# Performance work log

Hardware: AMD Instinct MI355X
Metric: run time of the kernel (lower is better)

## Reference

```python
import jax, jax.numpy as jnp
import numpy as np

B_SZ, T, IN_DIM, N_STATES, OUT_DIM = 64, 1024, 256, 512, 256


def setup_inputs() -> dict:
    key = jax.random.key(0)
    ks = jax.random.split(key, 5)
    def g(k, shp, sc):
        return jax.random.normal(k, shp, dtype=jnp.float32) * sc
    return {
        "x": g(ks[0], (B_SZ, T, IN_DIM), 1.0),
        "A": g(ks[1], (N_STATES, N_STATES), 1.0 / np.sqrt(N_STATES)),
        "Bm": g(ks[2], (IN_DIM, N_STATES), 1.0 / np.sqrt(IN_DIM)),
        "b": jnp.zeros((N_STATES,), jnp.float32),
        "C": g(ks[3], (N_STATES, OUT_DIM), 1.0 / np.sqrt(N_STATES)),
        "c": jnp.zeros((OUT_DIM,), jnp.float32),
        "D": g(ks[4], (N_STATES, OUT_DIM), 1.0 / np.sqrt(N_STATES)),
        "d": jnp.zeros((OUT_DIM,), jnp.float32),
    }


def reference(x, A, Bm, b, C, c, D, d):
    # x: [B, T, IN] -> time-major [T, B, IN] (mirrors tf.transpose perm=[1,0,2])
    xT = jnp.transpose(x, (1, 0, 2))
    s0 = jnp.zeros((x.shape[0], A.shape[0]), x.dtype)  # get_init_state: zeros [B, num_states]

    def step(state, xt):
        # nonlinear SSM cell: state update + Gaussian output params
        new_state = jnp.tanh(xt @ Bm + state @ A + b)
        loc = new_state @ C + c
        scale = jax.nn.softplus(new_state @ D + d)  # scale_diag > 0
        # emit stacked [2, B, OUT] (loc, scale) and the PRE-update state
        return new_state, (jnp.stack([loc, scale], axis=0), state)

    _, (ys, prev_states) = jax.lax.scan(step, s0, xT)
    # ys: [T, 2, B, OUT] -> [2, B, T, OUT] (tf perm [1,2,0,3])
    outputs = jnp.transpose(ys, (1, 2, 0, 3))
    state_out = prev_states[-1]  # state before the last cell update
    return outputs, state_out
```

## Files before the change

kernel.cpp:

```cpp
#include <hip/hip_runtime.h>
#include <hip/hip_bf16.h>
#include <cstdint>


typedef _Float16 f16;
typedef _Float16 f16x2 __attribute__((ext_vector_type(2)));
typedef _Float16 f16x4 __attribute__((ext_vector_type(4)));
typedef _Float16 f16x8 __attribute__((ext_vector_type(8)));
typedef float    f32x4 __attribute__((ext_vector_type(4)));

#define NS 512

#define OFF_S16   (0ull)
#define OFF_X16   (0ull)
#define OFF_U16   (67108864ull)
#define OFF_BMT   (134217728ull)
#define OFF_CDT   (134479872ull)
#define OFF_APREP (135004160ull)
#define OFF_ASTR  (135397376ull)

#if defined(__has_builtin)
#  if __has_builtin(__builtin_amdgcn_fdot2)
#    define HAS_FDOT2 1
#  endif
#endif

__device__ __forceinline__ float fdot2f(unsigned a, unsigned s, float c) {
#ifdef HAS_FDOT2
  return __builtin_amdgcn_fdot2(__builtin_bit_cast(f16x2, a),
                                __builtin_bit_cast(f16x2, s), c, false);
#else
  f16x2 av = __builtin_bit_cast(f16x2, a);
  f16x2 sv = __builtin_bit_cast(f16x2, s);
  return c + (float)av[0] * (float)sv[0] + (float)av[1] * (float)sv[1];
#endif
}

__device__ __forceinline__ unsigned packh2(float a, float b) {
  f16x2 h; h[0] = (f16)a; h[1] = (f16)b;
  return __builtin_bit_cast(unsigned, h);
}


__global__ void ck_x(const float* __restrict__ xg, f16* __restrict__ x16) {
  int i = (blockIdx.x * 256 + threadIdx.x) * 4;
  float4 v = *(const float4*)(xg + i);
  f16x4 h; h[0] = (f16)v.x; h[1] = (f16)v.y; h[2] = (f16)v.z; h[3] = (f16)v.w;
  *(f16x4*)(x16 + i) = h;
}

__global__ void ck_bmt(const float* __restrict__ Bm, f16* __restrict__ BmT) {
  int g = blockIdx.x * 256 + threadIdx.x;
  int n = g >> 8, k = g & 255;
  BmT[g] = (f16)Bm[k * 512 + n];
}

__global__ void ck_cdt(const float* __restrict__ C, const float* __restrict__ D,
                       f16* __restrict__ CDT) {
  int g = blockIdx.x * 256 + threadIdx.x;
  int n = g >> 9, k = g & 511;
  float v = (n < 256) ? C[k * 256 + n] : D[k * 256 + (n - 256)];
  CDT[g] = (f16)v;
}

__global__ void ck_a(const float* __restrict__ Ag, unsigned* __restrict__ Aprep,
                     unsigned* __restrict__ Astr) {
  int g = blockIdx.x * 256 + threadIdx.x;
  if (g < 98304) {
    int t = g / 192, rr = g % 192;
    int p = rr >> 3, jj = rr & 7;
    int kb = t >> 6, l = t & 63;
    int r0 = kb * 64 + 2 * p;
    int j = jj * 64 + l;
    Aprep[g] = packh2(Ag[r0 * 512 + j], Ag[(r0 + 1) * 512 + j]);
  } else {
    int q = g - 98304;
    int F = q >> 2, d = q & 3;
    int t = F & 511, f = F >> 9;
    int pp = f >> 1, jj2 = f & 1;
    int jj = jj2 * 4 + d;
    int kb = t >> 6, l = t & 63;
    int r0 = kb * 64 + 48 + 2 * pp;
    int j = jj * 64 + l;
    Astr[q] = packh2(Ag[r0 * 512 + j], Ag[(r0 + 1) * 512 + j]);
  }
}

template <int KDIM, int MODE>
__global__ __launch_bounds__(256, 2) void gemm_kernel(
    const f16* __restrict__ Ag, const f16* __restrict__ Bt,
    const float* __restrict__ bias0, const float* __restrict__ bias1,
    void* __restrict__ outp) {
  __shared__ f16 At[128 * 40];
  __shared__ f16 Bs[128 * 40];
  const int tid = threadIdx.x;
  const int m0 = blockIdx.y * 128;
  const int n0 = blockIdx.x * 128;
  const int w = tid >> 6, lane = tid & 63;
  const int wm = w & 1, wn = w >> 1;
  const int r = lane & 15, qd = lane >> 4;

  f32x4 zero4 = {0.f, 0.f, 0.f, 0.f};
  f32x4 acc[4][4];
#pragma unroll
  for (int mt = 0; mt < 4; ++mt)
#pragma unroll
    for (int nt = 0; nt < 4; ++nt) acc[mt][nt] = zero4;

  for (int kk = 0; kk < KDIM; kk += 32) {
#pragma unroll
    for (int s = 0; s < 2; ++s) {
      int fi = tid * 2 + s;
      int row = fi >> 2, q = fi & 3;
      float4 av = *(const float4*)(Ag + (size_t)(m0 + row) * KDIM + kk + q * 8);
      *(float4*)(At + row * 40 + q * 8) = av;
      float4 bv = *(const float4*)(Bt + (size_t)(n0 + row) * KDIM + kk + q * 8);
      *(float4*)(Bs + row * 40 + q * 8) = bv;
    }
    __syncthreads();
    f16x8 af[4], bf[4];
#pragma unroll
    for (int mt = 0; mt < 4; ++mt)
      af[mt] = *(const f16x8*)(At + (wm * 64 + mt * 16 + r) * 40 + qd * 8);
#pragma unroll
    for (int nt = 0; nt < 4; ++nt)
      bf[nt] = *(const f16x8*)(Bs + (wn * 64 + nt * 16 + r) * 40 + qd * 8);
#pragma unroll
    for (int mt = 0; mt < 4; ++mt)
#pragma unroll
      for (int nt = 0; nt < 4; ++nt)
        acc[mt][nt] = __builtin_amdgcn_mfma_f32_16x16x32_f16(af[mt], bf[nt],
                                                             acc[mt][nt], 0, 0, 0);
    __syncthreads();
  }

#pragma unroll
  for (int mt = 0; mt < 4; ++mt) {
#pragma unroll
    for (int nt = 0; nt < 4; ++nt) {
      int n = n0 + wn * 64 + nt * 16 + r;
#pragma unroll
      for (int i = 0; i < 4; ++i) {
        int m = m0 + wm * 64 + mt * 16 + qd * 4 + i;
        float v = acc[mt][nt][i];
        if (MODE == 0) {
          ((f16*)outp)[(size_t)m * NS + n] = (f16)(v + bias0[n]);
        } else {
          if (n < 256) {
            ((float*)outp)[(size_t)m * 256 + n] = v + bias0[n];
          } else {
            float z = v + bias1[n - 256];
            float sp = (z > 20.f) ? z : log1pf(__expf(z));
            ((float*)outp)[16777216ull + (size_t)m * 256 + (n - 256)] = sp;
          }
        }
      }
    }
  }
}


#define BCU(x) __builtin_bit_cast(unsigned, (x))

#define REGDOT(P, SC)                                   \
  do {                                                  \
    unsigned sb_ = BCU(SC);                             \
    float4 a0_ = areg[(P) * 2], a1_ = areg[(P) * 2 + 1];\
    acc0 = fdot2f(BCU(a0_.x), sb_, acc0);               \
    acc1 = fdot2f(BCU(a0_.y), sb_, acc1);               \
    acc2 = fdot2f(BCU(a0_.z), sb_, acc2);               \
    acc3 = fdot2f(BCU(a0_.w), sb_, acc3);               \
    acc4 = fdot2f(BCU(a1_.x), sb_, acc4);               \
    acc5 = fdot2f(BCU(a1_.y), sb_, acc5);               \
    acc6 = fdot2f(BCU(a1_.z), sb_, acc6);               \
    acc7 = fdot2f(BCU(a1_.w), sb_, acc7);               \
  } while (0)

#define GAPDOT(LO, HI, SC)                              \
  do {                                                  \
    unsigned sb_ = BCU(SC);                             \
    acc0 = fdot2f(BCU((LO).x), sb_, acc0);              \
    acc1 = fdot2f(BCU((LO).y), sb_, acc1);              \
    acc2 = fdot2f(BCU((LO).z), sb_, acc2);              \
    acc3 = fdot2f(BCU((LO).w), sb_, acc3);              \
    acc4 = fdot2f(BCU((HI).x), sb_, acc4);              \
    acc5 = fdot2f(BCU((HI).y), sb_, acc5);              \
    acc6 = fdot2f(BCU((HI).z), sb_, acc6);              \
    acc7 = fdot2f(BCU((HI).w), sb_, acc7);              \
  } while (0)

__global__ __launch_bounds__(512, 2) void scan_kernel(
    const float4* __restrict__ Aprep4, const float4* __restrict__ Astr4,
    const f16* __restrict__ U16, f16* __restrict__ S16,
    float* __restrict__ stout) {
  __shared__ float part[4096];
  __shared__ __align__(16) unsigned sf16[256];
  const int t = threadIdx.x;
  const int b = blockIdx.x;
  const int kb = t >> 6;

  float4 areg[48];
#pragma unroll
  for (int i = 0; i < 48; ++i) areg[i] = Aprep4[t * 48 + i];

  if (t < 256) sf16[t] = 0u;
  __syncthreads();

  const float4* sp4 = (const float4*)sf16;

#pragma unroll 1
  for (int ts = 0; ts < 1024; ++ts) {
    int zoff;
    asm volatile("s_mov_b32 %0, 0" : "=s"(zoff));
    const float4* astr = Astr4 + zoff;

    const int row = b * 1024 + ts;
    f16 uh = U16[(size_t)row * 512 + t];

    float4 gA0 = astr[0 * 512 + t], gA1 = astr[1 * 512 + t];
    float4 gA2 = astr[2 * 512 + t], gA3 = astr[3 * 512 + t];
    float4 gA4 = astr[4 * 512 + t], gA5 = astr[5 * 512 + t];
    float4 gA6 = astr[6 * 512 + t], gA7 = astr[7 * 512 + t];

    float acc0 = 0.f, acc1 = 0.f, acc2 = 0.f, acc3 = 0.f;
    float acc4 = 0.f, acc5 = 0.f, acc6 = 0.f, acc7 = 0.f;

#pragma unroll
    for (int c = 0; c < 6; ++c) {
      float4 s4 = sp4[kb * 8 + c];
      REGDOT(c * 4 + 0, s4.x);
      REGDOT(c * 4 + 1, s4.y);
      REGDOT(c * 4 + 2, s4.z);
      REGDOT(c * 4 + 3, s4.w);
    }

    float4 s4a = sp4[kb * 8 + 6], s4b = sp4[kb * 8 + 7];
    GAPDOT(gA0, gA1, s4a.x);
    GAPDOT(gA2, gA3, s4a.y);
    GAPDOT(gA4, gA5, s4a.z);
    GAPDOT(gA6, gA7, s4a.w);
    gA0 = astr[8 * 512 + t];  gA1 = astr[9 * 512 + t];
    gA2 = astr[10 * 512 + t]; gA3 = astr[11 * 512 + t];
    gA4 = astr[12 * 512 + t]; gA5 = astr[13 * 512 + t];
    gA6 = astr[14 * 512 + t]; gA7 = astr[15 * 512 + t];
    GAPDOT(gA0, gA1, s4b.x);
    GAPDOT(gA2, gA3, s4b.y);
    GAPDOT(gA4, gA5, s4b.z);
    GAPDOT(gA6, gA7, s4b.w);

    {
      const int l = t & 63;
      part[kb * 512 + 0 * 64 + l] = acc0;
      part[kb * 512 + 1 * 64 + l] = acc1;
      part[kb * 512 + 2 * 64 + l] = acc2;
      part[kb * 512 + 3 * 64 + l] = acc3;
      part[kb * 512 + 4 * 64 + l] = acc4;
      part[kb * 512 + 5 * 64 + l] = acc5;
      part[kb * 512 + 6 * 64 + l] = acc6;
      part[kb * 512 + 7 * 64 + l] = acc7;
    }
    __syncthreads();

    float sum = (float)uh;
#pragma unroll
    for (int k2 = 0; k2 < 8; ++k2) sum += part[k2 * 512 + t];
    float e = __expf(2.f * sum);
    float ns = 1.f - 2.f / (e + 1.f);

    S16[(size_t)row * 512 + t] = (f16)ns;
    if (ts == 1022) stout[b * 512 + t] = ns;

    float pn = __shfl_xor(ns, 1, 64);
    if (!(t & 1)) sf16[t >> 1] = packh2(ns, pn);
    __syncthreads();
  }
}


extern "C" void kernel_launch(void* const* d_in, const int* in_sizes, int n_in,
                              void* d_out, int out_size, void* d_ws, size_t ws_size,
                              hipStream_t stream) {
  (void)in_sizes; (void)n_in; (void)out_size; (void)ws_size;
  const float* xg  = (const float*)d_in[0];
  const float* Ag  = (const float*)d_in[1];
  const float* Bmg = (const float*)d_in[2];
  const float* bg  = (const float*)d_in[3];
  const float* Cg  = (const float*)d_in[4];
  const float* cg  = (const float*)d_in[5];
  const float* Dg  = (const float*)d_in[6];
  const float* dg  = (const float*)d_in[7];

  char* w = (char*)d_ws;
  f16* x16 = (f16*)(w + OFF_X16);
  f16* U16 = (f16*)(w + OFF_U16);
  f16* S16 = (f16*)(w + OFF_S16);
  f16* BmT = (f16*)(w + OFF_BMT);
  f16* CDT = (f16*)(w + OFF_CDT);
  unsigned* Aprep = (unsigned*)(w + OFF_APREP);
  unsigned* Astr  = (unsigned*)(w + OFF_ASTR);
  float* out = (float*)d_out;

  ck_x  <<<16384, 256, 0, stream>>>(xg, x16);
  ck_bmt<<<  512, 256, 0, stream>>>(Bmg, BmT);
  ck_cdt<<< 1024, 256, 0, stream>>>(Cg, Dg, CDT);
  ck_a  <<<  512, 256, 0, stream>>>(Ag, Aprep, Astr);

  gemm_kernel<256, 0><<<dim3(4, 512), 256, 0, stream>>>(x16, BmT, bg, nullptr,
                                                        (void*)U16);
  scan_kernel<<<64, 512, 0, stream>>>((const float4*)Aprep, (const float4*)Astr,
                                      U16, S16, out + 33554432);
  gemm_kernel<512, 1><<<dim3(4, 512), 256, 0, stream>>>(S16, CDT, cg, dg,
                                                        (void*)out);
}
```

Before: 2.345 ms.

## Double scan block to 1024 threads, each computing four output columns

The recurrent scan kernel now runs 1024 threads per batch element instead of 512. Each thread owns 4 output columns over a 64-row K slice, so per-thread register-held A shrinks from 48 to 16 float4, and A is repacked to match. This halves the serial fdot2 chain per thread at each timestep. It also writes the state directly as f16 to shared memory and defers the global state store by one step, so that write overlaps the next step's work. The extra threads bring more barrier cost and more streamed-A global loads per step, and half the threads sit idle during the tanh epilogue.

```diff
diff --git a/kernel.cpp b/kernel.cpp
--- a/kernel.cpp
+++ b/kernel.cpp
@@ -17,7 +17,7 @@
 #define OFF_BMT   (134217728ull)
 #define OFF_CDT   (134479872ull)
 #define OFF_APREP (135004160ull)
-#define OFF_ASTR  (135397376ull)
+#define OFF_ASTR  (135266304ull)
 
 #if defined(__has_builtin)
 #  if __has_builtin(__builtin_amdgcn_fdot2)
@@ -66,24 +66,30 @@
 __global__ void ck_a(const float* __restrict__ Ag, unsigned* __restrict__ Aprep,
                      unsigned* __restrict__ Astr) {
   int g = blockIdx.x * 256 + threadIdx.x;
-  if (g < 98304) {
-    int t = g / 192, rr = g % 192;
-    int p = rr >> 3, jj = rr & 7;
-    int kb = t >> 6, l = t & 63;
-    int r0 = kb * 64 + 2 * p;
-    int j = jj * 64 + l;
-    Aprep[g] = packh2(Ag[r0 * 512 + j], Ag[(r0 + 1) * 512 + j]);
+  int kb, c, jj, p;
+  unsigned* dst;
+  int idx;
+  if (g < 65536) {
+    int t = g >> 6, r = g & 63;
+    int q = r >> 2, e = r & 3;
+    jj = q & 3;
+    int pg = q >> 2;
+    p = pg * 4 + e;
+    kb = t >> 7; c = t & 127;
+    dst = Aprep; idx = g;
   } else {
-    int q = g - 98304;
-    int F = q >> 2, d = q & 3;
-    int t = F & 511, f = F >> 9;
-    int pp = f >> 1, jj2 = f & 1;
-    int jj = jj2 * 4 + d;
-    int kb = t >> 6, l = t & 63;
-    int r0 = kb * 64 + 48 + 2 * pp;
-    int j = jj * 64 + l;
-    Astr[q] = packh2(Ag[r0 * 512 + j], Ag[(r0 + 1) * 512 + j]);
+    int q2 = g - 65536;
+    int f = q2 >> 12, rr = q2 & 4095;
+    int t = rr >> 2, e = rr & 3;
+    jj = f & 3;
+    int pg2 = f >> 2;
+    p = 16 + pg2 * 4 + e;
+    kb = t >> 7; c = t & 127;
+    dst = Astr; idx = q2;
   }
+  int j = jj * 128 + c;
+  int k0 = kb * 64 + 2 * p;
+  dst[idx] = packh2(Ag[k0 * 512 + j], Ag[(k0 + 1) * 512 + j]);
 }
 
 template <int KDIM, int MODE>
@@ -162,118 +168,111 @@
 
 #define BCU(x) __builtin_bit_cast(unsigned, (x))
 
-#define REGDOT(P, SC)                                   \
-  do {                                                  \
-    unsigned sb_ = BCU(SC);                             \
-    float4 a0_ = areg[(P) * 2], a1_ = areg[(P) * 2 + 1];\
-    acc0 = fdot2f(BCU(a0_.x), sb_, acc0);               \
-    acc1 = fdot2f(BCU(a0_.y), sb_, acc1);               \
-    acc2 = fdot2f(BCU(a0_.z), sb_, acc2);               \
-    acc3 = fdot2f(BCU(a0_.w), sb_, acc3);               \
-    acc4 = fdot2f(BCU(a1_.x), sb_, acc4);               \
-    acc5 = fdot2f(BCU(a1_.y), sb_, acc5);               \
-    acc6 = fdot2f(BCU(a1_.z), sb_, acc6);               \
-    acc7 = fdot2f(BCU(a1_.w), sb_, acc7);               \
+#define DOT4(A0, A1, A2, A3, SV)              \
+  do {                                        \
+    unsigned sb_ = BCU(SV);                   \
+    a0 = fdot2f(BCU(A0), sb_, a0);            \
+    a1 = fdot2f(BCU(A1), sb_, a1);            \
+    a2 = fdot2f(BCU(A2), sb_, a2);            \
+    a3 = fdot2f(BCU(A3), sb_, a3);            \
   } while (0)
 
-#define GAPDOT(LO, HI, SC)                              \
-  do {                                                  \
-    unsigned sb_ = BCU(SC);                             \
-    acc0 = fdot2f(BCU((LO).x), sb_, acc0);              \
-    acc1 = fdot2f(BCU((LO).y), sb_, acc1);              \
-    acc2 = fdot2f(BCU((LO).z), sb_, acc2);              \
-    acc3 = fdot2f(BCU((LO).w), sb_, acc3);              \
-    acc4 = fdot2f(BCU((HI).x), sb_, acc4);              \
-    acc5 = fdot2f(BCU((HI).y), sb_, acc5);              \
-    acc6 = fdot2f(BCU((HI).z), sb_, acc6);              \
-    acc7 = fdot2f(BCU((HI).w), sb_, acc7);              \
+#define DOT16(Q0, Q1, Q2, Q3, S4)             \
+  do {                                        \
+    DOT4((Q0).x, (Q1).x, (Q2).x, (Q3).x, (S4).x); \
+    DOT4((Q0).y, (Q1).y, (Q2).y, (Q3).y, (S4).y); \
+    DOT4((Q0).z, (Q1).z, (Q2).z, (Q3).z, (S4).z); \
+    DOT4((Q0).w, (Q1).w, (Q2).w, (Q3).w, (S4).w); \
   } while (0)
 
-__global__ __launch_bounds__(512, 2) void scan_kernel(
+__global__ __launch_bounds__(1024, 4) void scan_kernel(
     const float4* __restrict__ Aprep4, const float4* __restrict__ Astr4,
     const f16* __restrict__ U16, f16* __restrict__ S16,
     float* __restrict__ stout) {
   __shared__ float part[4096];
-  __shared__ __align__(16) unsigned sf16[256];
+  __shared__ __align__(16) f16 sh[512];
   const int t = threadIdx.x;
   const int b = blockIdx.x;
-  const int kb = t >> 6;
-
-  float4 areg[48];
-#pragma unroll
-  for (int i = 0; i < 48; ++i) areg[i] = Aprep4[t * 48 + i];
-
-  if (t < 256) sf16[t] = 0u;
+  const int kb = t >> 7;
+  const int c = t & 127;
+
+  float4 areg[16];
+#pragma unroll
+  for (int i = 0; i < 16; ++i) areg[i] = Aprep4[t * 16 + i];
+
+  if (t < 512) sh[t] = (f16)0.f;
   __syncthreads();
 
-  const float4* sp4 = (const float4*)sf16;
+  const float4* sp4 = (const float4*)sh;
+  float ns_prev = 0.f;
 
 #pragma unroll 1
   for (int ts = 0; ts < 1024; ++ts) {
     int zoff;
     asm volatile("s_mov_b32 %0, 0" : "=s"(zoff));
-    const float4* astr = Astr4 + zoff;
-
-    const int row = b * 1024 + ts;
-    f16 uh = U16[(size_t)row * 512 + t];
-
-    float4 gA0 = astr[0 * 512 + t], gA1 = astr[1 * 512 + t];
-    float4 gA2 = astr[2 * 512 + t], gA3 = astr[3 * 512 + t];
-    float4 gA4 = astr[4 * 512 + t], gA5 = astr[5 * 512 + t];
-    float4 gA6 = astr[6 * 512 + t], gA7 = astr[7 * 512 + t];
-
-    float acc0 = 0.f, acc1 = 0.f, acc2 = 0.f, acc3 = 0.f;
-    float acc4 = 0.f, acc5 = 0.f, acc6 = 0.f, acc7 = 0.f;
-
-#pragma unroll
-    for (int c = 0; c < 6; ++c) {
-      float4 s4 = sp4[kb * 8 + c];
-      REGDOT(c * 4 + 0, s4.x);
-      REGDOT(c * 4 + 1, s4.y);
-      REGDOT(c * 4 + 2, s4.z);
-      REGDOT(c * 4 + 3, s4.w);
-    }
-
-    float4 s4a = sp4[kb * 8 + 6], s4b = sp4[kb * 8 + 7];
-    GAPDOT(gA0, gA1, s4a.x);
-    GAPDOT(gA2, gA3, s4a.y);
-    GAPDOT(gA4, gA5, s4a.z);
-    GAPDOT(gA6, gA7, s4a.w);
-    gA0 = astr[8 * 512 + t];  gA1 = astr[9 * 512 + t];
-    gA2 = astr[10 * 512 + t]; gA3 = astr[11 * 512 + t];
-    gA4 = astr[12 * 512 + t]; gA5 = astr[13 * 512 + t];
-    gA6 = astr[14 * 512 + t]; gA7 = astr[15 * 512 + t];
-    GAPDOT(gA0, gA1, s4b.x);
-    GAPDOT(gA2, gA3, s4b.y);
-    GAPDOT(gA4, gA5, s4b.z);
-    GAPDOT(gA6, gA7, s4b.w);
+    const float4* astr = Astr4 + zoff + t;
+
+    f16 uh = (f16)0.f;
+    if (t < 512) {
+      if (ts) S16[(size_t)(b * 1024 + ts - 1) * 512 + t] = (f16)ns_prev;
+      uh = U16[(size_t)(b * 1024 + ts) * 512 + t];
+    }
+
+    float4 g0 = astr[0 * 1024], g1 = astr[1 * 1024];
+    float4 g2 = astr[2 * 1024], g3 = astr[3 * 1024];
+    float4 g4 = astr[4 * 1024], g5 = astr[5 * 1024];
+    float4 g6 = astr[6 * 1024], g7 = astr[7 * 1024];
+
+    float a0 = 0.f, a1 = 0.f, a2 = 0.f, a3 = 0.f;
+
+#pragma unroll
+    for (int pg = 0; pg < 4; ++pg) {
+      float4 s4 = sp4[kb * 8 + pg];
+      DOT16(areg[pg * 4 + 0], areg[pg * 4 + 1],
+            areg[pg * 4 + 2], areg[pg * 4 + 3], s4);
+    }
 
     {
-      const int l = t & 63;
-      part[kb * 512 + 0 * 64 + l] = acc0;
-      part[kb * 512 + 1 * 64 + l] = acc1;
-      part[kb * 512 + 2 * 64 + l] = acc2;
-      part[kb * 512 + 3 * 64 + l] = acc3;
-      part[kb * 512 + 4 * 64 + l] = acc4;
-      part[kb * 512 + 5 * 64 + l] = acc5;
-      part[kb * 512 + 6 * 64 + l] = acc6;
-      part[kb * 512 + 7 * 64 + l] = acc7;
-    }
+      float4 s4 = sp4[kb * 8 + 4];
+      DOT16(g0, g1, g2, g3, s4);
+    }
+    {
+      float4 s4 = sp4[kb * 8 + 5];
+      DOT16(g4, g5, g6, g7, s4);
+    }
+    g0 = astr[8 * 1024];  g1 = astr[9 * 1024];
+    g2 = astr[10 * 1024]; g3 = astr[11 * 1024];
+    g4 = astr[12 * 1024]; g5 = astr[13 * 1024];
+    g6 = astr[14 * 1024]; g7 = astr[15 * 1024];
+    {
+      float4 s4 = sp4[kb * 8 + 6];
+      DOT16(g0, g1, g2, g3, s4);
+    }
+    {
+      float4 s4 = sp4[kb * 8 + 7];
+      DOT16(g4, g5, g6, g7, s4);
+    }
+
+    part[kb * 512 + 0 * 128 + c] = a0;
+    part[kb * 512 + 1 * 128 + c] = a1;
+    part[kb * 512 + 2 * 128 + c] = a2;
+    part[kb * 512 + 3 * 128 + c] = a3;
     __syncthreads();
 
-    float sum = (float)uh;
-#pragma unroll
-    for (int k2 = 0; k2 < 8; ++k2) sum += part[k2 * 512 + t];
-    float e = __expf(2.f * sum);
-    float ns = 1.f - 2.f / (e + 1.f);
-
-    S16[(size_t)row * 512 + t] = (f16)ns;
-    if (ts == 1022) stout[b * 512 + t] = ns;
-
-    float pn = __shfl_xor(ns, 1, 64);
-    if (!(t & 1)) sf16[t >> 1] = packh2(ns, pn);
+    if (t < 512) {
+      float sum = (float)uh;
+#pragma unroll
+      for (int k2 = 0; k2 < 8; ++k2) sum += part[k2 * 512 + t];
+      float e = __expf(2.f * sum);
+      float ns = 1.f - 2.f / (e + 1.f);
+      sh[t] = (f16)ns;
+      ns_prev = ns;
+      if (ts == 1022) stout[b * 512 + t] = ns;
+    }
     __syncthreads();
   }
+
+  if (t < 512) S16[(size_t)(b * 1024 + 1023) * 512 + t] = (f16)ns_prev;
 }
 
 
@@ -307,8 +306,8 @@
 
   gemm_kernel<256, 0><<<dim3(4, 512), 256, 0, stream>>>(x16, BmT, bg, nullptr,
                                                         (void*)U16);
-  scan_kernel<<<64, 512, 0, stream>>>((const float4*)Aprep, (const float4*)Astr,
-                                      U16, S16, out + 33554432);
+  scan_kernel<<<64, 1024, 0, stream>>>((const float4*)Aprep, (const float4*)Astr,
+                                       U16, S16, out + 33554432);
   gemm_kernel<512, 1><<<dim3(4, 512), 256, 0, stream>>>(S16, CDT, cg, dg,
                                                         (void*)out);
 }
```

Result: slower. 2.923 ms (+24.6%).

## Split recurrent A matrix across LDS, registers and streamed global loads in scan

Applied to the files above, without the earlier changes.

The scan kernel's per-thread slice of A (64 rows × 8 columns in fp16 pairs) was held mostly in registers (48 float4) with 16 rows streamed from global. It is now split three ways: 12 rows live in a 96KB LDS copy, 24 rows in registers (24 float4), and 28 rows are streamed from global/L2 each step, with loads interleaved between dot-product groups to hide latency. The state is also stored as plain f16 in shared memory without the shuffle-and-pack step, and the S16 global store is deferred by one step. This aims to relieve register pressure and let more streamed loads overlap compute, at the cost of more LDS and global traffic per timestep.

```diff
diff --git a/kernel.cpp b/kernel.cpp
--- a/kernel.cpp
+++ b/kernel.cpp
@@ -17,7 +17,8 @@
 #define OFF_BMT   (134217728ull)
 #define OFF_CDT   (134479872ull)
 #define OFF_APREP (135004160ull)
-#define OFF_ASTR  (135397376ull)
+#define OFF_ALDS  (135200768ull)
+#define OFF_ASTR  (135299072ull)
 
 #if defined(__has_builtin)
 #  if __has_builtin(__builtin_amdgcn_fdot2)
@@ -64,25 +65,35 @@
 }
 
 __global__ void ck_a(const float* __restrict__ Ag, unsigned* __restrict__ Aprep,
-                     unsigned* __restrict__ Astr) {
+                     unsigned* __restrict__ Alds, unsigned* __restrict__ Astr) {
   int g = blockIdx.x * 256 + threadIdx.x;
-  if (g < 98304) {
-    int t = g / 192, rr = g % 192;
-    int p = rr >> 3, jj = rr & 7;
+  if (g < 24576) {
+    int F = g >> 2, d = g & 3;
+    int t = F & 511, q = F >> 9;
+    int pl = q >> 1, jj2 = q & 1;
     int kb = t >> 6, l = t & 63;
-    int r0 = kb * 64 + 2 * p;
+    int jj = jj2 * 4 + d;
+    int k0 = kb * 64 + 2 * pl;
     int j = jj * 64 + l;
-    Aprep[g] = packh2(Ag[r0 * 512 + j], Ag[(r0 + 1) * 512 + j]);
+    Alds[g] = packh2(Ag[k0 * 512 + j], Ag[(k0 + 1) * 512 + j]);
+  } else if (g < 73728) {
+    int h = g - 24576;
+    int t = h / 96, rr = h % 96;
+    int P = rr >> 3, jj = rr & 7;
+    int kb = t >> 6, l = t & 63;
+    int k0 = kb * 64 + 12 + 2 * P;
+    int j = jj * 64 + l;
+    Aprep[h] = packh2(Ag[k0 * 512 + j], Ag[(k0 + 1) * 512 + j]);
   } else {
-    int q = g - 98304;
-    int F = q >> 2, d = q & 3;
+    int q2 = g - 73728;
+    int F = q2 >> 2, d = q2 & 3;
     int t = F & 511, f = F >> 9;
     int pp = f >> 1, jj2 = f & 1;
+    int kb = t >> 6, l = t & 63;
     int jj = jj2 * 4 + d;
-    int kb = t >> 6, l = t & 63;
-    int r0 = kb * 64 + 48 + 2 * pp;
+    int k0 = kb * 64 + 36 + 2 * pp;
     int j = jj * 64 + l;
-    Astr[q] = packh2(Ag[r0 * 512 + j], Ag[(r0 + 1) * 512 + j]);
+    Astr[q2] = packh2(Ag[k0 * 512 + j], Ag[(k0 + 1) * 512 + j]);
   }
 }
 
@@ -190,75 +201,125 @@
   } while (0)
 
 __global__ __launch_bounds__(512, 2) void scan_kernel(
-    const float4* __restrict__ Aprep4, const float4* __restrict__ Astr4,
-    const f16* __restrict__ U16, f16* __restrict__ S16,
-    float* __restrict__ stout) {
+    const float4* __restrict__ Aprep4, const float4* __restrict__ Alds4,
+    const float4* __restrict__ Astr4, const f16* __restrict__ U16,
+    f16* __restrict__ S16, float* __restrict__ stout) {
+  __shared__ __align__(16) f16 ldsA[49152];
   __shared__ float part[4096];
-  __shared__ __align__(16) unsigned sf16[256];
+  __shared__ __align__(16) f16 sh[512];
   const int t = threadIdx.x;
   const int b = blockIdx.x;
   const int kb = t >> 6;
-
-  float4 areg[48];
-#pragma unroll
-  for (int i = 0; i < 48; ++i) areg[i] = Aprep4[t * 48 + i];
-
-  if (t < 256) sf16[t] = 0u;
+  const int l = t & 63;
+
+  float4* ldsA4 = (float4*)ldsA;
+#pragma unroll
+  for (int q = 0; q < 12; ++q) ldsA4[q * 512 + t] = Alds4[q * 512 + t];
+
+  float4 areg[24];
+#pragma unroll
+  for (int i = 0; i < 24; ++i) areg[i] = Aprep4[t * 24 + i];
+
+  sh[t] = (f16)0.f;
   __syncthreads();
 
-  const float4* sp4 = (const float4*)sf16;
+  const float4* sp4 = (const float4*)sh;
+  float ns_prev = 0.f;
 
 #pragma unroll 1
   for (int ts = 0; ts < 1024; ++ts) {
     int zoff;
     asm volatile("s_mov_b32 %0, 0" : "=s"(zoff));
-    const float4* astr = Astr4 + zoff;
+    const float4* astr = Astr4 + zoff + t;
 
     const int row = b * 1024 + ts;
+    if (ts) S16[(size_t)(row - 1) * 512 + t] = (f16)ns_prev;
     f16 uh = U16[(size_t)row * 512 + t];
 
-    float4 gA0 = astr[0 * 512 + t], gA1 = astr[1 * 512 + t];
-    float4 gA2 = astr[2 * 512 + t], gA3 = astr[3 * 512 + t];
-    float4 gA4 = astr[4 * 512 + t], gA5 = astr[5 * 512 + t];
-    float4 gA6 = astr[6 * 512 + t], gA7 = astr[7 * 512 + t];
+    float4 g0 = astr[0 * 512], g1 = astr[1 * 512];
+    float4 g2 = astr[2 * 512], g3 = astr[3 * 512];
+    float4 g4 = astr[4 * 512], g5 = astr[5 * 512];
+    float4 g6 = astr[6 * 512], g7 = astr[7 * 512];
 
     float acc0 = 0.f, acc1 = 0.f, acc2 = 0.f, acc3 = 0.f;
     float acc4 = 0.f, acc5 = 0.f, acc6 = 0.f, acc7 = 0.f;
 
-#pragma unroll
-    for (int c = 0; c < 6; ++c) {
-      float4 s4 = sp4[kb * 8 + c];
-      REGDOT(c * 4 + 0, s4.x);
-      REGDOT(c * 4 + 1, s4.y);
-      REGDOT(c * 4 + 2, s4.z);
-      REGDOT(c * 4 + 3, s4.w);
-    }
-
-    float4 s4a = sp4[kb * 8 + 6], s4b = sp4[kb * 8 + 7];
-    GAPDOT(gA0, gA1, s4a.x);
-    GAPDOT(gA2, gA3, s4a.y);
-    GAPDOT(gA4, gA5, s4a.z);
-    GAPDOT(gA6, gA7, s4a.w);
-    gA0 = astr[8 * 512 + t];  gA1 = astr[9 * 512 + t];
-    gA2 = astr[10 * 512 + t]; gA3 = astr[11 * 512 + t];
-    gA4 = astr[12 * 512 + t]; gA5 = astr[13 * 512 + t];
-    gA6 = astr[14 * 512 + t]; gA7 = astr[15 * 512 + t];
-    GAPDOT(gA0, gA1, s4b.x);
-    GAPDOT(gA2, gA3, s4b.y);
-    GAPDOT(gA4, gA5, s4b.z);
-    GAPDOT(gA6, gA7, s4b.w);
-
-    {
-      const int l = t & 63;
-      part[kb * 512 + 0 * 64 + l] = acc0;
-      part[kb * 512 + 1 * 64 + l] = acc1;
-      part[kb * 512 + 2 * 64 + l] = acc2;
-      part[kb * 512 + 3 * 64 + l] = acc3;
-      part[kb * 512 + 4 * 64 + l] = acc4;
-      part[kb * 512 + 5 * 64 + l] = acc5;
-      part[kb * 512 + 6 * 64 + l] = acc6;
-      part[kb * 512 + 7 * 64 + l] = acc7;
-    }
+    {
+      float4 s4 = sp4[kb * 8 + 0];
+      float4 L0 = ldsA4[0 * 512 + t], L1 = ldsA4[1 * 512 + t];
+      float4 L2 = ldsA4[2 * 512 + t], L3 = ldsA4[3 * 512 + t];
+      float4 L4 = ldsA4[4 * 512 + t], L5 = ldsA4[5 * 512 + t];
+      float4 L6 = ldsA4[6 * 512 + t], L7 = ldsA4[7 * 512 + t];
+      GAPDOT(L0, L1, s4.x);
+      GAPDOT(L2, L3, s4.y);
+      GAPDOT(L4, L5, s4.z);
+      GAPDOT(L6, L7, s4.w);
+    }
+    {
+      float4 s4 = sp4[kb * 8 + 1];
+      float4 L8 = ldsA4[8 * 512 + t],  L9  = ldsA4[9 * 512 + t];
+      float4 L10 = ldsA4[10 * 512 + t], L11 = ldsA4[11 * 512 + t];
+      GAPDOT(L8, L9, s4.x);
+      GAPDOT(L10, L11, s4.y);
+      REGDOT(0, s4.z);
+      REGDOT(1, s4.w);
+    }
+
+    float4 h0 = astr[8 * 512],  h1 = astr[9 * 512];
+    float4 h2 = astr[10 * 512], h3 = astr[11 * 512];
+    float4 h4 = astr[12 * 512], h5 = astr[13 * 512];
+    float4 h6 = astr[14 * 512], h7 = astr[15 * 512];
+
+    {
+      float4 s4 = sp4[kb * 8 + 2];
+      REGDOT(2, s4.x); REGDOT(3, s4.y); REGDOT(4, s4.z); REGDOT(5, s4.w);
+    }
+    {
+      float4 s4 = sp4[kb * 8 + 3];
+      REGDOT(6, s4.x); REGDOT(7, s4.y); REGDOT(8, s4.z); REGDOT(9, s4.w);
+    }
+    {
+      float4 s4 = sp4[kb * 8 + 4];
+      REGDOT(10, s4.x); REGDOT(11, s4.y);
+      GAPDOT(g0, g1, s4.z);
+      GAPDOT(g2, g3, s4.w);
+    }
+    {
+      float4 s4 = sp4[kb * 8 + 5];
+      GAPDOT(g4, g5, s4.x);
+      GAPDOT(g6, g7, s4.y);
+      g0 = astr[16 * 512]; g1 = astr[17 * 512];
+      g2 = astr[18 * 512]; g3 = astr[19 * 512];
+      g4 = astr[20 * 512]; g5 = astr[21 * 512];
+      g6 = astr[22 * 512]; g7 = astr[23 * 512];
+      GAPDOT(h0, h1, s4.z);
+      GAPDOT(h2, h3, s4.w);
+    }
+    {
+      float4 s4 = sp4[kb * 8 + 6];
+      GAPDOT(h4, h5, s4.x);
+      GAPDOT(h6, h7, s4.y);
+      h0 = astr[24 * 512]; h1 = astr[25 * 512];
+      h2 = astr[26 * 512]; h3 = astr[27 * 512];
+      GAPDOT(g0, g1, s4.z);
+      GAPDOT(g2, g3, s4.w);
+    }
+    {
+      float4 s4 = sp4[kb * 8 + 7];
+      GAPDOT(g4, g5, s4.x);
+      GAPDOT(g6, g7, s4.y);
+      GAPDOT(h0, h1, s4.z);
+      GAPDOT(h2, h3, s4.w);
+    }
+
+    part[kb * 512 + 0 * 64 + l] = acc0;
+    part[kb * 512 + 1 * 64 + l] = acc1;
+    part[kb * 512 + 2 * 64 + l] = acc2;
+    part[kb * 512 + 3 * 64 + l] = acc3;
+    part[kb * 512 + 4 * 64 + l] = acc4;
+    part[kb * 512 + 5 * 64 + l] = acc5;
+    part[kb * 512 + 6 * 64 + l] = acc6;
+    part[kb * 512 + 7 * 64 + l] = acc7;
     __syncthreads();
 
     float sum = (float)uh;
@@ -267,13 +328,13 @@
     float e = __expf(2.f * sum);
     float ns = 1.f - 2.f / (e + 1.f);
 
-    S16[(size_t)row * 512 + t] = (f16)ns;
+    sh[t] = (f16)ns;
+    ns_prev = ns;
     if (ts == 1022) stout[b * 512 + t] = ns;
-
-    float pn = __shfl_xor(ns, 1, 64);
-    if (!(t & 1)) sf16[t >> 1] = packh2(ns, pn);
     __syncthreads();
   }
+
+  S16[(size_t)(b * 1024 + 1023) * 512 + t] = (f16)ns_prev;
 }
 
 
@@ -297,18 +358,20 @@
   f16* BmT = (f16*)(w + OFF_BMT);
   f16* CDT = (f16*)(w + OFF_CDT);
   unsigned* Aprep = (unsigned*)(w + OFF_APREP);
+  unsigned* Alds  = (unsigned*)(w + OFF_ALDS);
   unsigned* Astr  = (unsigned*)(w + OFF_ASTR);
   float* out = (float*)d_out;
 
   ck_x  <<<16384, 256, 0, stream>>>(xg, x16);
   ck_bmt<<<  512, 256, 0, stream>>>(Bmg, BmT);
   ck_cdt<<< 1024, 256, 0, stream>>>(Cg, Dg, CDT);
-  ck_a  <<<  512, 256, 0, stream>>>(Ag, Aprep, Astr);
+  ck_a  <<<  512, 256, 0, stream>>>(Ag, Aprep, Alds, Astr);
 
   gemm_kernel<256, 0><<<dim3(4, 512), 256, 0, stream>>>(x16, BmT, bg, nullptr,
                                                         (void*)U16);
-  scan_kernel<<<64, 512, 0, stream>>>((const float4*)Aprep, (const float4*)Astr,
-                                      U16, S16, out + 33554432);
+  scan_kernel<<<64, 512, 0, stream>>>((const float4*)Aprep, (const float4*)Alds,
+                                      (const float4*)Astr, U16, S16,
+                                      out + 33554432);
   gemm_kernel<512, 1><<<dim3(4, 512), 256, 0, stream>>>(S16, CDT, cg, dg,
                                                         (void*)out);
 }
```

Measured after the change: 2.549 ms. +8.7%, slower.
